# Kernel tuning notes

Measured on AMD Instinct MI355X. Metric: run time of the kernel, lower is better.

## Reference

```python
import jax, jax.numpy as jnp
import numpy as np
from jax.scipy.special import logsumexp

B, L, M, D = 8192, 1024, 128, 2  # batch, hilbert.size, bond dim, local_size
MACHINE_POW = 2


def setup_inputs() -> dict:
    key = jax.random.key(0)
    k1, k2 = jax.random.split(key)
    # configurations in the zero-magnetization sector: each row is a permutation
    # of L//2 zeros and L//2 ones (constrained HomogeneousHilbert)
    base = jnp.tile(jnp.arange(D, dtype=jnp.int32), L // D)  # (L,)
    inputs = jax.vmap(lambda k: jax.random.permutation(k, base))(jax.random.split(k1, B))
    # variational parameters epsilon: (local_size, M, size); centered at 1 so the
    # length-L multiplicative cache chain stays in fp32 range
    epsilon = 1.0 + 0.02 * jax.random.normal(k2, (D, M, L), dtype=jnp.float32)
    return {"inputs": inputs, "epsilon": epsilon}


def _conditionals(inputs, epsilon):
    # inputs: (B, L) int in [0, D); epsilon: (D, M, L)
    Bn, Ln = inputs.shape
    Dn, Mn, _ = epsilon.shape
    half = Ln // 2

    def scan_fun(carry, index):
        cache, n_spins = carry                       # (B, D, M), (B, D)
        prev = inputs[:, (index - 1) % Ln]           # (B,) previous-site state
        params_i = epsilon[:, :, index]              # (D, M)
        # irregular gather: cache[b, prev[b], :]
        gathered = jnp.take_along_axis(cache, prev[:, None, None], axis=1)[:, 0, :]  # (B, M)
        prods = params_i[None, :, :] * gathered[:, None, :]  # (B, D, M)
        log_psi = jnp.sum(prods, axis=-1)            # (B, D) sum over bond dim
        n_spins = jnp.where(index > 0,
                            n_spins + jax.nn.one_hot(prev, Dn, dtype=jnp.int32),
                            n_spins)
        # zero-magnetization renormalization: -inf once a local state is exhausted
        renorm = jnp.log(jnp.heaviside((half - n_spins).astype(log_psi.dtype), 0.0))
        return (prods, n_spins), log_psi + renorm

    cache0 = jnp.ones((Bn, Dn, Mn), epsilon.dtype)
    n0 = jnp.zeros((Bn, Dn), jnp.int32)
    _, log_psi = jax.lax.scan(scan_fun, (cache0, n0), jnp.arange(Ln))
    return jnp.transpose(log_psi, (1, 0, 2))  # (B, L, D)


def reference(inputs, epsilon):
    lp = _conditionals(inputs, epsilon)  # (B, L, D)
    # normalize conditionals over local states (machine_pow = 2)
    lp = lp - (1.0 / MACHINE_POW) * logsumexp(MACHINE_POW * lp, axis=-1, keepdims=True)
    # pick the log-conditional of the actual configuration at each site
    sel = jnp.take_along_axis(lp, inputs[:, :, None], axis=2)[:, :, 0]  # (B, L)
    # n_symm = 1 (default apply_symmetries): symmetrized logsumexp is identity
    return jnp.sum(sel, axis=1)  # (B,) log_psi
```

## Files before the change

### kernel.cpp

```cpp
#include <hip/hip_runtime.h>
#include <hip/hip_fp16.h>

typedef unsigned long long u64;
typedef unsigned int uint32;
typedef short short8 __attribute__((ext_vector_type(8)));
typedef float f32x4 __attribute__((ext_vector_type(4)));
typedef _Float16 h2 __attribute__((ext_vector_type(2)));

#define B_N 8192
#define L_N 1024
#define M_N 128
#define C_N 16
#define CH_N 64
#define HALF_N 512

#define OFF_W16  0
#define OFF_R16  0x40000
#define OFF_BITS 0x80000
#define OFF_LR   0x180000
#define OFF_RQ   0x1C0000
#define OFF_T    0x21C0000

#define PACK_BLK (B_N * L_N / 256)
#define EPS_BLK  32
#define ZERO_BLK 32

__device__ __forceinline__ unsigned short f32_bf16(float f) {
    union { float f; unsigned u; } x; x.f = f;
    unsigned u = x.u + 0x7FFFu + ((x.u >> 16) & 1u);
    return (unsigned short)(u >> 16);
}

__device__ __forceinline__ float fdot2(h2 a, h2 b, float c) {
#if __has_builtin(__builtin_amdgcn_fdot2)
    return __builtin_amdgcn_fdot2(a, b, c, false);
#else
    return (float)a[0] * (float)b[0] + (float)a[1] * (float)b[1] + c;
#endif
}

__global__ __launch_bounds__(256) void k_prep(const int* __restrict__ inp,
        const float* __restrict__ eps, u64* __restrict__ bits,
        _Float16* __restrict__ w16, _Float16* __restrict__ r16,
        unsigned short* __restrict__ lrT, float* __restrict__ out) {
    int bid = blockIdx.x;
    if (bid < PACK_BLK) {
        int g = bid * 256 + threadIdx.x;
        int v = inp[g];
        u64 m = __ballot(v != 0);
        if ((threadIdx.x & 63) == 0) bits[g >> 6] = m;
        return;
    }
    bid -= PACK_BLK;
    if (bid < EPS_BLK) {
        int wid = threadIdx.x >> 6, lane = threadIdx.x & 63;
        int m = bid * 4 + wid;
        const float* e0 = eps + (size_t)m * L_N + lane * 16;
        const float* e1 = eps + (size_t)(M_N + m) * L_N + lane * 16;
        float a[16], b[16];
        #pragma unroll
        for (int j = 0; j < 16; j += 4) {
            *(float4*)&a[j] = *(const float4*)&e0[j];
            *(float4*)&b[j] = *(const float4*)&e1[j];
        }
        float local = 1.f;
        #pragma unroll
        for (int j = 0; j < 16; ++j) local *= a[j];
        float sc = local;
        #pragma unroll
        for (int d = 1; d < 64; d <<= 1) {
            float up = __shfl_up(sc, d);
            if (lane >= d) sc *= up;
        }
        float prev = __shfl_up(sc, 1);
        float E = (lane == 0) ? 1.f : prev;
        int i0 = lane * 16;
        #pragma unroll
        for (int j = 0; j < 16; ++j) {
            float rat = b[j] / a[j];
            w16[(size_t)(i0 + j) * M_N + m] = (_Float16)(E * (a[j] - b[j]));
            r16[(size_t)(i0 + j) * M_N + m] = (_Float16)rat;
            lrT[(size_t)m * L_N + i0 + j] = f32_bf16(__log2f(rat));
            E *= a[j];
        }
        return;
    }
    bid -= EPS_BLK;
    if (bid < ZERO_BLK) {
        out[bid * 256 + threadIdx.x] = 0.f;
    }
}

__global__ __launch_bounds__(256) void k_slog2(const u64* __restrict__ bits,
        const unsigned short* __restrict__ lrT, _Float16* __restrict__ Rq,
        int* __restrict__ T) {
    if (blockIdx.x >= 1024) {
        int b = (blockIdx.x - 1024) * 256 + threadIdx.x;
        const u64* brow = bits + (size_t)b * 16;
        int n1 = 0, n0 = 0, Tv = 1024;
        for (int wd = 0; wd < 16; ++wd) {
            u64 x = brow[wd];
            int pc = __popcll(x);
            if (n1 + pc < HALF_N && n0 + (64 - pc) < HALF_N) {
                n1 += pc; n0 += 64 - pc;
                continue;
            }
            int found = 0;
            for (int k = 0; k < 64; ++k) {
                if (n1 >= HALF_N || n0 >= HALF_N) { Tv = wd * 64 + k; found = 1; break; }
                int sb = (int)((x >> k) & 1);
                n1 += sb; n0 += 1 - sb;
            }
            if (!found) Tv = (wd + 1) * 64;
            break;
        }
        T[b] = Tv;
        return;
    }
    int btile = blockIdx.x >> 1;
    int half = blockIdx.x & 1;
    int wid = threadIdx.x >> 6, lane = threadIdx.x & 63;
    int col = lane & 15, quad = lane >> 4;
    int m = (half * 4 + wid) * 16 + col;
    int b_row = btile * 16 + col;
    const u64* brow = bits + (size_t)b_row * 16;
    const unsigned short* lrow = lrT + (size_t)m * L_N;

    f32x4 cum = (f32x4){0.f, 0.f, 0.f, 0.f};

    for (int c = 0; c < C_N; ++c) {
        #pragma unroll
        for (int reg = 0; reg < 4; ++reg) {
            int b = btile * 16 + quad * 4 + reg;
            Rq[((size_t)c * B_N + b) * M_N + m] = (_Float16)exp2f(cum[reg]);
        }
        u64 wv = brow[c];
        short8 a0, a1;
        #pragma unroll
        for (int j = 0; j < 8; ++j) {
            a0[j] = (short)((((wv >> (quad * 8 + j)) & 1) != 0) ? 0x3F80 : 0);
            a1[j] = (short)((((wv >> (32 + quad * 8 + j)) & 1) != 0) ? 0x3F80 : 0);
        }
        const unsigned short* bp = lrow + c * 64 + quad * 8;
        union { uint4 u; short8 s; } bf0, bf1;
        bf0.u = *(const uint4*)bp;
        bf1.u = *(const uint4*)(bp + 32);
        cum = __builtin_amdgcn_mfma_f32_16x16x32_bf16(a0, bf0.s, cum, 0, 0, 0);
        cum = __builtin_amdgcn_mfma_f32_16x16x32_bf16(a1, bf1.s, cum, 0, 0, 0);
    }
}

__global__ __launch_bounds__(256, 2) void k_main(const u64* __restrict__ bits,
        const _Float16* __restrict__ w16, const _Float16* __restrict__ r16,
        const _Float16* __restrict__ Rq, const int* __restrict__ T,
        float* __restrict__ out) {
    __shared__ _Float16 wbuf[CH_N * M_N];
    __shared__ _Float16 rbuf[CH_N * M_N];
    int c = blockIdx.x & (C_N - 1);
    int bblk = blockIdx.x >> 4;
    int lane = threadIdx.x & 63, wid = threadIdx.x >> 6;
    int s = lane & 7, g = lane >> 3;
    int b0 = bblk * 128 + wid * 32 + g * 4;
    int b_own = b0 + (s & 3);

    {
        const uint4* sw = (const uint4*)(w16 + (size_t)c * CH_N * M_N);
        const uint4* sr = (const uint4*)(r16 + (size_t)c * CH_N * M_N);
        uint4* dw = (uint4*)wbuf; uint4* dr = (uint4*)rbuf;
        #pragma unroll
        for (int t = 0; t < 4; ++t) {
            dw[threadIdx.x + t * 256] = sw[threadIdx.x + t * 256];
            dr[threadIdx.x + t * 256] = sr[threadIdx.x + t * 256];
        }
    }

    h2 R2[4][8];
    #pragma unroll
    for (int nb = 0; nb < 4; ++nb) {
        union { uint4 q[2]; h2 h[8]; } P;
        const uint4* src = (const uint4*)(Rq + ((size_t)c * B_N + (b0 + nb)) * M_N + s * 16);
        P.q[0] = src[0]; P.q[1] = src[1];
        #pragma unroll
        for (int j = 0; j < 8; ++j) R2[nb][j] = P.h[j];
    }
    int Tb = T[b_own];
    u64 wb[4];
    #pragma unroll
    for (int nb = 0; nb < 4; ++nb) wb[nb] = bits[(size_t)(b0 + nb) * 16 + c];

    __syncthreads();

    const h2 one2 = (h2){(_Float16)1.f, (_Float16)1.f};
    float sum = 0.f;
    #pragma unroll
    for (int h = 0; h < 2; ++h) {
        uint32 wh[4];
        #pragma unroll
        for (int nb = 0; nb < 4; ++nb) wh[nb] = (uint32)(wb[nb] >> (h * 32));
        uint32 owa = (s & 1) ? wh[1] : wh[0];
        uint32 owb = (s & 1) ? wh[3] : wh[2];
        uint32 ow = (s & 2) ? owb : owa;

        int rel = Tb - (c * CH_N + h * 32);
        uint32 vmask = (rel <= 0) ? 0u : ((rel >= 32) ? 0xFFFFFFFFu : ((1u << rel) - 1u));

        for (int tt = 0; tt < 32; ++tt) {
            int base = (h * 32 + tt) * M_N + s * 16;
            union { uint4 q[2]; h2 h[8]; } W, Rr;
            W.q[0] = *(const uint4*)&wbuf[base];
            W.q[1] = *((const uint4*)&wbuf[base] + 1);
            Rr.q[0] = *(const uint4*)&rbuf[base];
            Rr.q[1] = *((const uint4*)&rbuf[base] + 1);

            float d[4];
            #pragma unroll
            for (int nb = 0; nb < 4; ++nb) {
                float acc = 0.f;
                #pragma unroll
                for (int j = 0; j < 8; ++j) acc = fdot2(R2[nb][j], W.h[j], acc);
                d[nb] = acc;
            }
            float xa = (s & 1) ? d[1] : d[0];
            float ya = (s & 1) ? d[0] : d[1];
            xa += __shfl_xor(ya, 1);
            float xb = (s & 1) ? d[3] : d[2];
            float yb = (s & 1) ? d[2] : d[3];
            xb += __shfl_xor(yb, 1);
            float u2 = (s & 2) ? xb : xa;
            float v2 = (s & 2) ? xa : xb;
            u2 += __shfl_xor(v2, 2);
            u2 += __shfl_xor(u2, 4);
            float Dv = u2;

            int sbit = (ow >> tt) & 1;
            float y = sbit ? Dv : -Dv;
            float contr = -0.5f * __logf(1.f + __expf(2.f * y));
            sum += ((vmask >> tt) & 1) ? contr : 0.f;

            #pragma unroll
            for (int nb = 0; nb < 4; ++nb) {
                bool bit = (wh[nb] >> tt) & 1;
                #pragma unroll
                for (int j = 0; j < 8; ++j) {
                    h2 sel = bit ? Rr.h[j] : one2;
                    R2[nb][j] *= sel;
                }
            }
        }
    }
    if (s < 4) atomicAdd(&out[b_own], sum);
}

extern "C" void kernel_launch(void* const* d_in, const int* in_sizes, int n_in,
                              void* d_out, int out_size, void* d_ws, size_t ws_size,
                              hipStream_t stream) {
    const int*   inputs  = (const int*)d_in[0];
    const float* epsilon = (const float*)d_in[1];
    float* out = (float*)d_out;

    char* ws = (char*)d_ws;
    _Float16* w16 = (_Float16*)(ws + OFF_W16);
    _Float16* r16 = (_Float16*)(ws + OFF_R16);
    u64*   bits   = (u64*)  (ws + OFF_BITS);
    unsigned short* lrT = (unsigned short*)(ws + OFF_LR);
    _Float16* Rq  = (_Float16*)(ws + OFF_RQ);
    int*   T      = (int*)  (ws + OFF_T);

    k_prep<<<PACK_BLK + EPS_BLK + ZERO_BLK, 256, 0, stream>>>(
        inputs, epsilon, bits, w16, r16, lrT, out);
    k_slog2<<<1024 + 32, 256, 0, stream>>>(bits, lrT, Rq, T);
    k_main<<<(B_N / 128) * C_N, 256, 0, stream>>>(bits, w16, r16, Rq, T, out);
}
```

Measured before the change: 186.0 us.

## Process two sites per step using precomputed pair correction and combined ratio tables

The main loop now advances two sites per iteration. It precomputes a per-pair correction vector (w*(r0-1)), so the second site's dot product is formed from the un-updated state plus a correction instead of waiting on the multiplicative update. It also precomputes the product of two ratios, so the state is multiplied at most once per pair and only when a bit is set. This shortens the serial dependency chain and skips the multiplications where the bit is zero, at the cost of a third dot product per pair, extra LDS tables and branchy control flow. The launch-bounds occupancy hint of 2 was dropped.

```diff
diff --git a/kernel.cpp b/kernel.cpp
--- a/kernel.cpp
+++ b/kernel.cpp
@@ -18,8 +18,10 @@
 #define OFF_R16  0x40000
 #define OFF_BITS 0x80000
 #define OFF_LR   0x180000
-#define OFF_RQ   0x1C0000
-#define OFF_T    0x21C0000
+#define OFF_WC   0x1C0000
+#define OFF_U3   0x1E0000
+#define OFF_RQ   0x200000
+#define OFF_T    0x2200000
 
 #define PACK_BLK (B_N * L_N / 256)
 #define EPS_BLK  32
@@ -42,6 +44,7 @@
 __global__ __launch_bounds__(256) void k_prep(const int* __restrict__ inp,
         const float* __restrict__ eps, u64* __restrict__ bits,
         _Float16* __restrict__ w16, _Float16* __restrict__ r16,
+        _Float16* __restrict__ wc16, _Float16* __restrict__ u316,
         unsigned short* __restrict__ lrT, float* __restrict__ out) {
     int bid = blockIdx.x;
     if (bid < PACK_BLK) {
@@ -75,12 +78,21 @@
         float prev = __shfl_up(sc, 1);
         float E = (lane == 0) ? 1.f : prev;
         int i0 = lane * 16;
+        float rat0 = 1.f;
         #pragma unroll
         for (int j = 0; j < 16; ++j) {
             float rat = b[j] / a[j];
-            w16[(size_t)(i0 + j) * M_N + m] = (_Float16)(E * (a[j] - b[j]));
+            float wval = E * (a[j] - b[j]);
+            w16[(size_t)(i0 + j) * M_N + m] = (_Float16)wval;
             r16[(size_t)(i0 + j) * M_N + m] = (_Float16)rat;
             lrT[(size_t)m * L_N + i0 + j] = f32_bf16(__log2f(rat));
+            if (j & 1) {
+                int p = (i0 + j) >> 1;
+                wc16[(size_t)p * M_N + m] = (_Float16)(wval * (rat0 - 1.f));
+                u316[(size_t)p * M_N + m] = (_Float16)(rat0 * rat);
+            } else {
+                rat0 = rat;
+            }
             E *= a[j];
         }
         return;
@@ -150,27 +162,38 @@
     }
 }
 
-__global__ __launch_bounds__(256, 2) void k_main(const u64* __restrict__ bits,
+__global__ __launch_bounds__(256) void k_main(const u64* __restrict__ bits,
         const _Float16* __restrict__ w16, const _Float16* __restrict__ r16,
+        const _Float16* __restrict__ wc16, const _Float16* __restrict__ u316,
         const _Float16* __restrict__ Rq, const int* __restrict__ T,
         float* __restrict__ out) {
     __shared__ _Float16 wbuf[CH_N * M_N];
     __shared__ _Float16 rbuf[CH_N * M_N];
+    __shared__ _Float16 wcbuf[(CH_N / 2) * M_N];
+    __shared__ _Float16 u3buf[(CH_N / 2) * M_N];
     int c = blockIdx.x & (C_N - 1);
     int bblk = blockIdx.x >> 4;
     int lane = threadIdx.x & 63, wid = threadIdx.x >> 6;
     int s = lane & 7, g = lane >> 3;
-    int b0 = bblk * 128 + wid * 32 + g * 4;
-    int b_own = b0 + (s & 3);
+    int b0i = bblk * 128 + wid * 32 + g * 4;
+    int b_own = b0i + (s & 3);
 
     {
         const uint4* sw = (const uint4*)(w16 + (size_t)c * CH_N * M_N);
         const uint4* sr = (const uint4*)(r16 + (size_t)c * CH_N * M_N);
+        const uint4* sc_ = (const uint4*)(wc16 + (size_t)c * (CH_N / 2) * M_N);
+        const uint4* su = (const uint4*)(u316 + (size_t)c * (CH_N / 2) * M_N);
         uint4* dw = (uint4*)wbuf; uint4* dr = (uint4*)rbuf;
+        uint4* dc = (uint4*)wcbuf; uint4* du = (uint4*)u3buf;
         #pragma unroll
         for (int t = 0; t < 4; ++t) {
             dw[threadIdx.x + t * 256] = sw[threadIdx.x + t * 256];
             dr[threadIdx.x + t * 256] = sr[threadIdx.x + t * 256];
+        }
+        #pragma unroll
+        for (int t = 0; t < 2; ++t) {
+            dc[threadIdx.x + t * 256] = sc_[threadIdx.x + t * 256];
+            du[threadIdx.x + t * 256] = su[threadIdx.x + t * 256];
         }
     }
 
@@ -178,7 +201,7 @@
     #pragma unroll
     for (int nb = 0; nb < 4; ++nb) {
         union { uint4 q[2]; h2 h[8]; } P;
-        const uint4* src = (const uint4*)(Rq + ((size_t)c * B_N + (b0 + nb)) * M_N + s * 16);
+        const uint4* src = (const uint4*)(Rq + ((size_t)c * B_N + (b0i + nb)) * M_N + s * 16);
         P.q[0] = src[0]; P.q[1] = src[1];
         #pragma unroll
         for (int j = 0; j < 8; ++j) R2[nb][j] = P.h[j];
@@ -186,11 +209,10 @@
     int Tb = T[b_own];
     u64 wb[4];
     #pragma unroll
-    for (int nb = 0; nb < 4; ++nb) wb[nb] = bits[(size_t)(b0 + nb) * 16 + c];
+    for (int nb = 0; nb < 4; ++nb) wb[nb] = bits[(size_t)(b0i + nb) * 16 + c];
 
     __syncthreads();
 
-    const h2 one2 = (h2){(_Float16)1.f, (_Float16)1.f};
     float sum = 0.f;
     #pragma unroll
     for (int h = 0; h < 2; ++h) {
@@ -204,46 +226,84 @@
         int rel = Tb - (c * CH_N + h * 32);
         uint32 vmask = (rel <= 0) ? 0u : ((rel >= 32) ? 0xFFFFFFFFu : ((1u << rel) - 1u));
 
-        for (int tt = 0; tt < 32; ++tt) {
-            int base = (h * 32 + tt) * M_N + s * 16;
-            union { uint4 q[2]; h2 h[8]; } W, Rr;
-            W.q[0] = *(const uint4*)&wbuf[base];
-            W.q[1] = *((const uint4*)&wbuf[base] + 1);
-            Rr.q[0] = *(const uint4*)&rbuf[base];
-            Rr.q[1] = *((const uint4*)&rbuf[base] + 1);
-
-            float d[4];
+        for (int pp = 0; pp < 16; ++pp) {
+            int tt0 = 2 * pp;
+            int rowi = h * 32 + tt0;
+            int prow = h * 16 + pp;
+            union { uint4 q[2]; h2 h[8]; } W0, W1, WC;
+            {
+                const uint4* p0 = (const uint4*)&wbuf[rowi * M_N + s * 16];
+                W0.q[0] = p0[0]; W0.q[1] = p0[1];
+                const uint4* p1 = (const uint4*)&wbuf[(rowi + 1) * M_N + s * 16];
+                W1.q[0] = p1[0]; W1.q[1] = p1[1];
+                const uint4* pc = (const uint4*)&wcbuf[prow * M_N + s * 16];
+                WC.q[0] = pc[0]; WC.q[1] = pc[1];
+            }
+
+            float pA[4], pD1[4];
             #pragma unroll
             for (int nb = 0; nb < 4; ++nb) {
-                float acc = 0.f;
+                float aA = 0.f, aB = 0.f, aC = 0.f;
                 #pragma unroll
-                for (int j = 0; j < 8; ++j) acc = fdot2(R2[nb][j], W.h[j], acc);
-                d[nb] = acc;
-            }
-            float xa = (s & 1) ? d[1] : d[0];
-            float ya = (s & 1) ? d[0] : d[1];
-            xa += __shfl_xor(ya, 1);
-            float xb = (s & 1) ? d[3] : d[2];
-            float yb = (s & 1) ? d[2] : d[3];
-            xb += __shfl_xor(yb, 1);
-            float u2 = (s & 2) ? xb : xa;
-            float v2 = (s & 2) ? xa : xb;
-            u2 += __shfl_xor(v2, 2);
-            u2 += __shfl_xor(u2, 4);
-            float Dv = u2;
-
-            int sbit = (ow >> tt) & 1;
-            float y = sbit ? Dv : -Dv;
-            float contr = -0.5f * __logf(1.f + __expf(2.f * y));
-            sum += ((vmask >> tt) & 1) ? contr : 0.f;
+                for (int j = 0; j < 8; ++j) {
+                    aA = fdot2(R2[nb][j], W0.h[j], aA);
+                    aB = fdot2(R2[nb][j], W1.h[j], aB);
+                    aC = fdot2(R2[nb][j], WC.h[j], aC);
+                }
+                int bitn = (wh[nb] >> tt0) & 1;
+                float bc = aB + aC;
+                pA[nb] = aA;
+                pD1[nb] = bitn ? bc : aB;
+            }
+            float DA, D1;
+            {
+                float xa = (s & 1) ? pA[1] : pA[0];
+                float ya = (s & 1) ? pA[0] : pA[1];
+                xa += __shfl_xor(ya, 1);
+                float xb = (s & 1) ? pA[3] : pA[2];
+                float yb = (s & 1) ? pA[2] : pA[3];
+                xb += __shfl_xor(yb, 1);
+                float u2 = (s & 2) ? xb : xa;
+                float v2 = (s & 2) ? xa : xb;
+                u2 += __shfl_xor(v2, 2);
+                u2 += __shfl_xor(u2, 4);
+                DA = u2;
+            }
+            {
+                float xa = (s & 1) ? pD1[1] : pD1[0];
+                float ya = (s & 1) ? pD1[0] : pD1[1];
+                xa += __shfl_xor(ya, 1);
+                float xb = (s & 1) ? pD1[3] : pD1[2];
+                float yb = (s & 1) ? pD1[2] : pD1[3];
+                xb += __shfl_xor(yb, 1);
+                float u2 = (s & 2) ? xb : xa;
+                float v2 = (s & 2) ? xa : xb;
+                u2 += __shfl_xor(v2, 2);
+                u2 += __shfl_xor(u2, 4);
+                D1 = u2;
+            }
+
+            int s0 = (ow >> tt0) & 1;
+            int s1 = (ow >> (tt0 + 1)) & 1;
+            float y0 = s0 ? DA : -DA;
+            float y1 = s1 ? D1 : -D1;
+            float c0 = -0.5f * __logf(1.f + __expf(2.f * y0));
+            float c1 = -0.5f * __logf(1.f + __expf(2.f * y1));
+            sum += ((vmask >> tt0) & 1) ? c0 : 0.f;
+            sum += ((vmask >> (tt0 + 1)) & 1) ? c1 : 0.f;
 
             #pragma unroll
             for (int nb = 0; nb < 4; ++nb) {
-                bool bit = (wh[nb] >> tt) & 1;
-                #pragma unroll
-                for (int j = 0; j < 8; ++j) {
-                    h2 sel = bit ? Rr.h[j] : one2;
-                    R2[nb][j] *= sel;
+                int v = (int)((wh[nb] >> tt0) & 3u);
+                if (v) {
+                    const _Float16* src = (v == 3)
+                        ? &u3buf[prow * M_N + s * 16]
+                        : &rbuf[(rowi + (v >> 1)) * M_N + s * 16];
+                    union { uint4 q[2]; h2 h[8]; } U;
+                    U.q[0] = *(const uint4*)src;
+                    U.q[1] = *((const uint4*)src + 1);
+                    #pragma unroll
+                    for (int j = 0; j < 8; ++j) R2[nb][j] *= U.h[j];
                 }
             }
         }
@@ -263,11 +323,13 @@
     _Float16* r16 = (_Float16*)(ws + OFF_R16);
     u64*   bits   = (u64*)  (ws + OFF_BITS);
     unsigned short* lrT = (unsigned short*)(ws + OFF_LR);
+    _Float16* wc16 = (_Float16*)(ws + OFF_WC);
+    _Float16* u316 = (_Float16*)(ws + OFF_U3);
     _Float16* Rq  = (_Float16*)(ws + OFF_RQ);
     int*   T      = (int*)  (ws + OFF_T);
 
     k_prep<<<PACK_BLK + EPS_BLK + ZERO_BLK, 256, 0, stream>>>(
-        inputs, epsilon, bits, w16, r16, lrT, out);
+        inputs, epsilon, bits, w16, r16, wc16, u316, lrT, out);
     k_slog2<<<1024 + 32, 256, 0, stream>>>(bits, lrT, Rq, T);
-    k_main<<<(B_N / 128) * C_N, 256, 0, stream>>>(bits, w16, r16, Rq, T, out);
-}
+    k_main<<<(B_N / 128) * C_N, 256, 0, stream>>>(bits, w16, r16, wc16, u316, Rq, T, out);
+}
```

Result: slower. 197.2 us (+6.1%).
